# Optimization experiments

Hardware: AMD Instinct MI355X
Metric: run time of the kernel (lower is better)

The kernel has to match this reference:

```python
import jax, jax.numpy as jnp
import numpy as np

B, DIM = 64, 131072


def setup_inputs() -> dict:
    key = jax.random.key(0)
    k1, k2, k3 = jax.random.split(key, 3)
    z = jax.random.normal(k1, (B, DIM), dtype=jnp.float32)
    trace_in = jax.random.normal(k2, (B, DIM), dtype=jnp.float32)
    ctrl = jax.random.normal(k3, (B, 3), dtype=jnp.float32)
    return {"z": z, "trace_in": trace_in, "ctrl": ctrl}


def reference(z, trace_in, ctrl):
    # gates: [B,1]
    store = jax.nn.sigmoid(ctrl[:, 0:1])
    retrieve = jax.nn.sigmoid(ctrl[:, 1:2])
    # clear gate only touches the internal buffer (no effect on outputs); omitted.

    # global max-abs normalization (single scalar, as in torch: z.abs().max())
    z_norm = z / (jnp.abs(z).max() + 1e-6)

    z_f = jnp.fft.fft(z_norm)          # [B,DIM] complex64
    trace_f = jnp.fft.fft(trace_in)    # [B,DIM] complex64
    new_trace_f = trace_f + z_f * store
    new_trace = jnp.fft.ifft(new_trace_f)
    read = jnp.fft.ifft(new_trace_f * jnp.conj(z_f)) * retrieve

    dummy_ptr = jnp.zeros((z.shape[0], 1), dtype=jnp.float32)
    return (read, new_trace, dummy_ptr, jnp.array(1.0, dtype=jnp.float32))
```

## Files before the change

### kernel.cpp

```cpp
#include <hip/hip_runtime.h>
#include <math.h>

#define NROW 64
#define DIM  131072

struct cf { float x, y; };
__device__ __forceinline__ cf cadd(cf a, cf b){ return {a.x+b.x, a.y+b.y}; }
__device__ __forceinline__ cf csub(cf a, cf b){ return {a.x-b.x, a.y-b.y}; }
__device__ __forceinline__ cf cmul(cf a, cf b){ return {a.x*b.x - a.y*b.y, a.x*b.y + a.y*b.x}; }
template<int SG> __device__ __forceinline__ cf muli(cf a){
  return (SG > 0) ? cf{-a.y, a.x} : cf{a.y, -a.x};
}
__device__ __forceinline__ float sigmoidf(float x){ return 1.0f/(1.0f + __expf(-x)); }

__device__ __forceinline__ void wsync(){
  __builtin_amdgcn_wave_barrier();
  asm volatile("" ::: "memory");
}

typedef float __attribute__((ext_vector_type(4))) fvec4;
typedef float __attribute__((ext_vector_type(2))) fvec2;

template<int SG> __device__ __forceinline__ void fft4(cf&a0, cf&a1, cf&a2, cf&a3){
  cf e0=cadd(a0,a2), e1=csub(a0,a2), o0=cadd(a1,a3), o1=csub(a1,a3);
  cf w=muli<SG>(o1);
  a0=cadd(e0,o0); a2=csub(e0,o0); a1=cadd(e1,w); a3=csub(e1,w);
}

template<int SG> __device__ __forceinline__ void fft8(cf v[8]){
  cf e0=v[0], e1=v[2], e2=v[4], e3=v[6];
  cf o0=v[1], o1=v[3], o2=v[5], o3=v[7];
  fft4<SG>(e0,e1,e2,e3); fft4<SG>(o0,o1,o2,o3);
  const float R=0.70710678118654752f;
  cf w1=cmul(o1, cf{R, (float)SG*R});
  cf w2=muli<SG>(o2);
  cf w3=cmul(o3, cf{-R, (float)SG*R});
  v[0]=cadd(e0,o0); v[4]=csub(e0,o0);
  v[1]=cadd(e1,w1); v[5]=csub(e1,w1);
  v[2]=cadd(e2,w2); v[6]=csub(e2,w2);
  v[3]=cadd(e3,w3); v[7]=csub(e3,w3);
}

template<int SG> __device__ __forceinline__ void fft16(cf v[16]){
  cf e[8], o[8];
  #pragma unroll
  for(int i=0;i<8;i++){ e[i]=v[2*i]; o[i]=v[2*i+1]; }
  fft8<SG>(e); fft8<SG>(o);
  const float C[8]={1.f,0.92387953251128674f,0.70710678118654752f,0.38268343236508977f,
                    0.f,-0.38268343236508977f,-0.70710678118654752f,-0.92387953251128674f};
  const float S[8]={0.f,0.38268343236508977f,0.70710678118654752f,0.92387953251128674f,
                    1.f,0.92387953251128674f,0.70710678118654752f,0.38268343236508977f};
  #pragma unroll
  for(int k=0;k<8;k++){
    cf w=cmul(o[k], cf{C[k], (float)SG*S[k]});
    v[k]=cadd(e[k],w); v[k+8]=csub(e[k],w);
  }
}

__global__ void k0_tail(float* __restrict__ dout, int cplx){
  int t = threadIdx.x;
  size_t base = (size_t)2*NROW*DIM*cplx;
  if(t < NROW) dout[base + t] = 0.f;
  else if(t == NROW) dout[base + NROW] = 1.0f;
}

__global__ __launch_bounds__(256) void k1_maxabs(const float* __restrict__ z, unsigned* __restrict__ dst){
  __shared__ float red[256];
  size_t i0 = (size_t)blockIdx.x*blockDim.x + threadIdx.x;
  size_t stride = (size_t)gridDim.x*blockDim.x;
  const float4* z4 = (const float4*)z;
  size_t n4 = (size_t)NROW*DIM/4;
  float m = 0.f;
  for(size_t i=i0;i<n4;i+=stride){
    float4 v=z4[i];
    m = fmaxf(m, fmaxf(fmaxf(fabsf(v.x),fabsf(v.y)), fmaxf(fabsf(v.z),fabsf(v.w))));
  }
  red[threadIdx.x]=m; __syncthreads();
  #pragma unroll
  for(int s=128;s>0;s>>=1){
    if(threadIdx.x<(unsigned)s) red[threadIdx.x]=fmaxf(red[threadIdx.x],red[threadIdx.x+s]);
    __syncthreads();
  }
  if(threadIdx.x==0) atomicMax(dst, __float_as_uint(red[0]));
}

__global__ __launch_bounds__(256) void k2_fwd1(
    const float* __restrict__ z, const float* __restrict__ tr,
    const float* __restrict__ ctrl, const unsigned* __restrict__ maxbits,
    float2* __restrict__ Bws, float* __restrict__ out_nt, int cplx)
{
  __shared__ float reb[4384], imb[4384];
  __shared__ float twc[256], tws[256];
  int t = threadIdx.x;
  int b = blockIdx.x >> 5;
  int n1b = (blockIdx.x & 31) << 4;
  {
    float sv, cv;
    __sincosf(-0.0245436926061703f * (float)t, &sv, &cv);
    twc[t]=cv; tws[t]=sv;
  }
  float s = 1.0f/(__uint_as_float(*maxbits) + 1e-6f);
  float gs = sigmoidf(ctrl[b*3+0]);
  float cc = gs*s;
  const float4* zr4 = (const float4*)(z  + (size_t)b*DIM);
  const float4* tr4 = (const float4*)(tr + (size_t)b*DIM);
  #pragma unroll
  for(int it=0; it<4; ++it){
    int e = t + 256*it;
    int n2 = e >> 2, j4 = e & 3;
    int fi = n2*128 + (n1b>>2) + j4;
    float4 zv = zr4[fi];
    float4 tv = tr4[fi];
    int lb = n2*17 + j4*4;
    reb[lb+0]=zv.x; reb[lb+1]=zv.y; reb[lb+2]=zv.z; reb[lb+3]=zv.w;
    imb[lb+0]=tv.x; imb[lb+1]=tv.y; imb[lb+2]=tv.z; imb[lb+3]=tv.w;
    float n0 = fmaf(cc, zv.x, tv.x);
    float n1v= fmaf(cc, zv.y, tv.y);
    float n2v= fmaf(cc, zv.z, tv.z);
    float n3 = fmaf(cc, zv.w, tv.w);
    size_t n = (size_t)n2*512 + n1b + j4*4;
    size_t oidx = (size_t)b*DIM + n;
    if(cplx == 2){
      fvec4 a  = {n0, 0.f, n1v, 0.f};
      fvec4 bq = {n2v, 0.f, n3, 0.f};
      fvec4* op = (fvec4*)((float2*)out_nt + oidx);
      __builtin_nontemporal_store(a,  op);
      __builtin_nontemporal_store(bq, op+1);
    } else {
      out_nt[oidx+0]=n0; out_nt[oidx+1]=n1v; out_nt[oidx+2]=n2v; out_nt[oidx+3]=n3;
    }
  }
  __syncthreads();
  int f = t & 15, p = t >> 4;
  cf v[16];
  #pragma unroll
  for(int q=0;q<16;q++){ int n2=q*16+p; v[q].x=reb[n2*17+f]; v[q].y=imb[n2*17+f]; }
  fft16<-1>(v);
  #pragma unroll
  for(int kq=1;kq<16;kq++){ int tt=(p*kq)&255; v[kq]=cmul(v[kq], cf{twc[tt], tws[tt]}); }
  __syncthreads();
  #pragma unroll
  for(int kq=0;kq<16;kq++){ reb[f*274 + kq*17 + p]=v[kq].x; imb[f*274 + kq*17 + p]=v[kq].y; }
  __syncthreads();
  #pragma unroll
  for(int pp=0;pp<16;pp++){ v[pp].x=reb[f*274 + p*17 + pp]; v[pp].y=imb[f*274 + p*17 + pp]; }
  fft16<-1>(v);
  int nn1 = n1b + f;
  cf w, st;
  {
    float sv, cv;
    __sincosf(-4.793689960382698e-05f * (float)(nn1*p), &sv, &cv);
    w = {cv, sv};
    __sincosf(-4.793689960382698e-05f * 16.f * (float)nn1, &sv, &cv);
    st = {cv, sv};
  }
  #pragma unroll
  for(int kp=0;kp<16;kp++){
    int k2 = kp*16 + p;
    cf r = cmul(v[kp], w);
    Bws[((size_t)b<<17) + (size_t)k2*512 + nn1] = make_float2(r.x, r.y);
    w = cmul(w, st);
  }
}

template<int SG>
__device__ __forceinline__ void fft512_block(
    float* Xre, float* Xim, float* Tre, float* Tim,
    int lane, const float* twc, const float* tws)
{
  cf v[8];
  #pragma unroll
  for(int q=0;q<8;q++){ v[q].x=Xre[q*64+lane]; v[q].y=Xim[q*64+lane]; }
  fft8<SG>(v);
  #pragma unroll
  for(int kq=1;kq<8;kq++){ int tt=(lane*kq)&511; v[kq]=cmul(v[kq], cf{twc[tt], (float)SG*tws[tt]}); }
  #pragma unroll
  for(int kq=0;kq<8;kq++){ Tre[lane*9+kq]=v[kq].x; Tim[lane*9+kq]=v[kq].y; }
  wsync();
  int kQ = lane>>3, pp = lane&7;
  #pragma unroll
  for(int q=0;q<8;q++){ int idx=(q*8+pp)*9+kQ; v[q].x=Tre[idx]; v[q].y=Tim[idx]; }
  fft8<SG>(v);
  #pragma unroll
  for(int kq=1;kq<8;kq++){ int tt=(pp*kq*8)&511; v[kq]=cmul(v[kq], cf{twc[tt], (float)SG*tws[tt]}); }
  wsync();
  #pragma unroll
  for(int kq=0;kq<8;kq++){ Xre[pp*73+kq*9+kQ]=v[kq].x; Xim[pp*73+kq*9+kQ]=v[kq].y; }
  wsync();
  #pragma unroll
  for(int p2=0;p2<8;p2++){ int idx=p2*73 + kQ*9 + pp; v[p2].x=Xre[idx]; v[p2].y=Xim[idx]; }
  fft8<SG>(v);
  #pragma unroll
  for(int kp=0;kp<8;kp++){ int k=kp*64 + kQ*8 + pp; Tre[k]=v[kp].x; Tim[k]=v[kp].y; }
  wsync();
}

__global__ __launch_bounds__(128) void k3_mid(
    float2* __restrict__ Bws, const float* __restrict__ ctrl,
    const unsigned* __restrict__ maxbits)
{
  __shared__ float Xs[4*584], Ts[4*584];
  __shared__ float twc[512], tws[512];
  int t = threadIdx.x;
  int b  = blockIdx.x >> 7;
  int pr = blockIdx.x & 127;
  int cA = (pr==0) ? 0   : pr;
  int cB = (pr==0) ? 128 : 256-pr;
  int col = t >> 6, lane = t & 63;
  int myc = col ? cB : cA;
  for(int i=t;i<512;i+=128){
    float sv,cv; __sincosf(0.0122718463030851f*(float)i, &sv, &cv);
    twc[i]=cv; tws[i]=sv;
  }
  float s = 1.0f/(__uint_as_float(*maxbits)+1e-6f);
  float gs = sigmoidf(ctrl[b*3+0]);
  float alpha = sigmoidf(ctrl[b*3+1]) * (1.0f/(float)DIM);
  float* Xre = Xs + (2*col)*584; float* Xim = Xre + 584;
  float* Tre = Ts + (2*col)*584; float* Tim = Tre + 584;
  float2* colp = Bws + ((size_t)b<<17) + ((size_t)myc<<9);
  const float4* colp4 = (const float4*)colp;
  #pragma unroll
  for(int r=0;r<4;r++){
    float4 q = colp4[lane + 64*r];
    int j = 2*(lane + 64*r);
    Xre[j]=q.x;   Xim[j]=q.y;
    Xre[j+1]=q.z; Xim[j+1]=q.w;
  }
  __syncthreads();
  fft512_block<-1>(Xre, Xim, Tre, Tim, lane, twc, tws);
  __syncthreads();
  const float* Pre = (pr==0) ? Tre : (Ts + (2*(1-col))*584);
  const float* Pim = Pre + 584;
  #pragma unroll
  for(int r=0;r<8;r++){
    int k1  = lane + 64*r;
    int k1p = (myc==0) ? ((512-k1)&511) : (511-k1);
    float cr = Tre[k1], ci = Tim[k1];
    float qr = Pre[k1p], qi = -Pim[k1p];
    float zur = 0.5f*(cr+qr), zui = 0.5f*(ci+qi);
    float dr = cr-qr, di = ci-qi;
    float tfr = 0.5f*di, tfi = -0.5f*dr;
    float szr = s*zur, szi = s*zui;
    float ntr = fmaf(gs, szr, tfr), nti = fmaf(gs, szi, tfi);
    float prr = (ntr*szr + nti*szi)*alpha;
    float pii = (nti*szr - ntr*szi)*alpha;
    Xre[k1]=prr; Xim[k1]=pii;
  }
  __syncthreads();
  fft512_block<1>(Xre, Xim, Tre, Tim, lane, twc, tws);
  cf w, st;
  {
    float sv,cv;
    __sincosf(4.793689960382698e-05f * (float)(lane*myc), &sv, &cv);
    w = {cv, sv};
    __sincosf(4.793689960382698e-05f * 64.f * (float)myc, &sv, &cv);
    st = {cv, sv};
  }
  #pragma unroll
  for(int r=0;r<8;r++){
    int m1 = lane + 64*r;
    cf r2 = cmul(cf{Tre[m1],Tim[m1]}, w);
    colp[m1] = make_float2(r2.x, r2.y);
    w = cmul(w, st);
  }
}

__global__ __launch_bounds__(256) void k4_inv2(
    const float2* __restrict__ Qws, float* __restrict__ dout, int cplx)
{
  __shared__ float reb[4384], imb[4384];
  __shared__ float twc[256], tws[256];
  int t = threadIdx.x;
  int b = blockIdx.x >> 5;
  int m1b = (blockIdx.x & 31) << 4;
  {
    float sv, cv;
    __sincosf(0.0245436926061703f * (float)t, &sv, &cv);
    twc[t]=cv; tws[t]=sv;
  }
  const float4* Qp = (const float4*)(Qws + ((size_t)b<<17));
  #pragma unroll
  for(int it=0; it<8; ++it){
    int e = t + 256*it;
    int k2 = e >> 3, j = e & 7;
    float4 q = Qp[k2*256 + (m1b>>1) + j];
    int lb = k2*17 + 2*j;
    reb[lb+0]=q.x; imb[lb+0]=q.y;
    reb[lb+1]=q.z; imb[lb+1]=q.w;
  }
  __syncthreads();
  int f = t & 15, p = t >> 4;
  cf v[16];
  #pragma unroll
  for(int q=0;q<16;q++){ int k2=q*16+p; v[q].x=reb[k2*17+f]; v[q].y=imb[k2*17+f]; }
  fft16<1>(v);
  #pragma unroll
  for(int kq=1;kq<16;kq++){ int tt=(p*kq)&255; v[kq]=cmul(v[kq], cf{twc[tt], tws[tt]}); }
  __syncthreads();
  #pragma unroll
  for(int kq=0;kq<16;kq++){ reb[f*274+kq*17+p]=v[kq].x; imb[f*274+kq*17+p]=v[kq].y; }
  __syncthreads();
  #pragma unroll
  for(int pp=0;pp<16;pp++){ v[pp].x=reb[f*274+p*17+pp]; v[pp].y=imb[f*274+p*17+pp]; }
  fft16<1>(v);
  #pragma unroll
  for(int kp=0;kp<16;kp++){
    int m2 = kp*16 + p;
    size_t n = (size_t)(m1b + f) + (size_t)512*m2;
    size_t oidx = (size_t)b*DIM + n;
    if(cplx==2){
      ((float2*)dout)[oidx] = make_float2(v[kp].x, 0.f);
    }
    else dout[oidx] = v[kp].x;
  }
}

extern "C" void kernel_launch(void* const* d_in, const int* in_sizes, int n_in,
                              void* d_out, int out_size, void* d_ws, size_t ws_size,
                              hipStream_t stream)
{
  (void)in_sizes; (void)n_in; (void)ws_size;
  const float* z    = (const float*)d_in[0];
  const float* tr   = (const float*)d_in[1];
  const float* ctrl = (const float*)d_in[2];
  float* dout = (float*)d_out;
  int cplx = (out_size > 20000000) ? 2 : 1;
  unsigned* maxbits = (unsigned*)d_ws;
  float2* Bws = (float2*)((char*)d_ws + 256);

  hipMemsetAsync(d_ws, 0, 4, stream);
  hipLaunchKernelGGL(k0_tail,  dim3(1),    dim3(128), 0, stream, dout, cplx);
  hipLaunchKernelGGL(k1_maxabs,dim3(1024), dim3(256), 0, stream, z, maxbits);
  hipLaunchKernelGGL(k2_fwd1,  dim3(2048), dim3(256), 0, stream,
                     z, tr, ctrl, maxbits, Bws, dout + (size_t)NROW*DIM*cplx, cplx);
  hipLaunchKernelGGL(k3_mid,   dim3(8192), dim3(128), 0, stream, Bws, ctrl, maxbits);
  hipLaunchKernelGGL(k4_inv2,  dim3(2048), dim3(256), 0, stream, Bws, dout, cplx);
}
```

Before: 217.7 us.

## Fuse FFT stages into persistent kernel with per-batch dependency counters

Replaces the three FFT-stage launches with one persistent kernel of 1024 blocks. Each block pulls tiles from an atomic work queue, and per-batch-row completion counters with acquire/release atomics let later stages start on a row as soon as its inputs are ready. This is meant to remove launch gaps and kernel-boundary drains and to overlap stages across rows. It also halves the twiddle table with a sign trick and packs two k3 columns-pairs per 256-thread block. The costs are spin-wait polling, a bounded spin that could proceed early, and shared memory sized for the largest stage, which may lower occupancy.

Measured after the change: 491.4 us. 2.26x slower.

```diff
diff --git a/kernel.cpp b/kernel.cpp
--- a/kernel.cpp
+++ b/kernel.cpp
@@ -3,6 +3,13 @@
 
 #define NROW 64
 #define DIM  131072
+
+#define NK2 2048
+#define NK3 4096
+#define NK4 2048
+#define T_K3 (NK2)
+#define T_K4 (NK2+NK3)
+#define NT_TOT (NK2+NK3+NK4)
 
 struct cf { float x, y; };
 __device__ __forceinline__ cf cadd(cf a, cf b){ return {a.x+b.x, a.y+b.y}; }
@@ -19,7 +26,6 @@
 }
 
 typedef float __attribute__((ext_vector_type(4))) fvec4;
-typedef float __attribute__((ext_vector_type(2))) fvec2;
 
 template<int SG> __device__ __forceinline__ void fft4(cf&a0, cf&a1, cf&a2, cf&a3){
   cf e0=cadd(a0,a2), e1=csub(a0,a2), o0=cadd(a1,a3), o1=csub(a1,a3);
@@ -84,16 +90,35 @@
   if(threadIdx.x==0) atomicMax(dst, __float_as_uint(red[0]));
 }
 
-__global__ __launch_bounds__(256) void k2_fwd1(
+__device__ __forceinline__ void wait_count(unsigned* p, unsigned need){
+  if(threadIdx.x==0){
+    unsigned v, tries = 0;
+    do {
+      v = __hip_atomic_load(p, __ATOMIC_RELAXED, __HIP_MEMORY_SCOPE_AGENT);
+      if(v >= need) break;
+      __builtin_amdgcn_s_sleep(8);
+    } while(++tries < (1u<<19));
+    (void)__hip_atomic_load(p, __ATOMIC_ACQUIRE, __HIP_MEMORY_SCOPE_AGENT);
+  }
+  __syncthreads();
+}
+__device__ __forceinline__ void signal_done(unsigned* p){
+  __syncthreads();
+  if(threadIdx.x==0)
+    (void)__hip_atomic_fetch_add(p, 1u, __ATOMIC_RELEASE, __HIP_MEMORY_SCOPE_AGENT);
+}
+
+
+__device__ __forceinline__ void k2_body(
+    float* __restrict__ S, unsigned tile,
     const float* __restrict__ z, const float* __restrict__ tr,
     const float* __restrict__ ctrl, const unsigned* __restrict__ maxbits,
     float2* __restrict__ Bws, float* __restrict__ out_nt, int cplx)
 {
-  __shared__ float reb[4384], imb[4384];
-  __shared__ float twc[256], tws[256];
+  float* reb = S; float* imb = S+4384; float* twc = S+8768; float* tws = S+9024;
   int t = threadIdx.x;
-  int b = blockIdx.x >> 5;
-  int n1b = (blockIdx.x & 31) << 4;
+  int b = tile >> 5;
+  int n1b = (tile & 31) << 4;
   {
     float sv, cv;
     __sincosf(-0.0245436926061703f * (float)t, &sv, &cv);
@@ -173,7 +198,10 @@
   for(int q=0;q<8;q++){ v[q].x=Xre[q*64+lane]; v[q].y=Xim[q*64+lane]; }
   fft8<SG>(v);
   #pragma unroll
-  for(int kq=1;kq<8;kq++){ int tt=(lane*kq)&511; v[kq]=cmul(v[kq], cf{twc[tt], (float)SG*tws[tt]}); }
+  for(int kq=1;kq<8;kq++){
+    int tt=(lane*kq)&511; int ti=tt&255; float sg=(tt&256)?-1.f:1.f;
+    v[kq]=cmul(v[kq], cf{sg*twc[ti], (float)SG*sg*tws[ti]});
+  }
   #pragma unroll
   for(int kq=0;kq<8;kq++){ Tre[lane*9+kq]=v[kq].x; Tim[lane*9+kq]=v[kq].y; }
   wsync();
@@ -182,7 +210,10 @@
   for(int q=0;q<8;q++){ int idx=(q*8+pp)*9+kQ; v[q].x=Tre[idx]; v[q].y=Tim[idx]; }
   fft8<SG>(v);
   #pragma unroll
-  for(int kq=1;kq<8;kq++){ int tt=(pp*kq*8)&511; v[kq]=cmul(v[kq], cf{twc[tt], (float)SG*tws[tt]}); }
+  for(int kq=1;kq<8;kq++){
+    int tt=(pp*kq*8)&511; int ti=tt&255; float sg=(tt&256)?-1.f:1.f;
+    v[kq]=cmul(v[kq], cf{sg*twc[ti], (float)SG*sg*tws[ti]});
+  }
   wsync();
   #pragma unroll
   for(int kq=0;kq<8;kq++){ Xre[pp*73+kq*9+kQ]=v[kq].x; Xim[pp*73+kq*9+kQ]=v[kq].y; }
@@ -195,45 +226,49 @@
   wsync();
 }
 
-__global__ __launch_bounds__(128) void k3_mid(
+__device__ __forceinline__ void k3_body(
+    float* __restrict__ S, unsigned r,
     float2* __restrict__ Bws, const float* __restrict__ ctrl,
     const unsigned* __restrict__ maxbits)
 {
-  __shared__ float Xs[4*584], Ts[4*584];
-  __shared__ float twc[512], tws[512];
   int t = threadIdx.x;
-  int b  = blockIdx.x >> 7;
-  int pr = blockIdx.x & 127;
+  int b   = r >> 6;
+  int idx = r & 63;
+  int wp  = t >> 7;
+  int tt  = t & 127;
+  int pr  = idx*2 + wp;
   int cA = (pr==0) ? 0   : pr;
   int cB = (pr==0) ? 128 : 256-pr;
-  int col = t >> 6, lane = t & 63;
+  int col = tt >> 6, lane = tt & 63;
   int myc = col ? cB : cA;
-  for(int i=t;i<512;i+=128){
-    float sv,cv; __sincosf(0.0122718463030851f*(float)i, &sv, &cv);
-    twc[i]=cv; tws[i]=sv;
+  int colid = wp*2 + col;
+  float* Xre = S + colid*1168;        float* Xim = Xre + 584;
+  float* Tre = S + 4672 + colid*1168; float* Tim = Tre + 584;
+  float* twc = S + 9344; float* tws = S + 9600;
+  if(t < 256){
+    float sv,cv; __sincosf(0.0122718463030851f*(float)t, &sv, &cv);
+    twc[t]=cv; tws[t]=sv;
   }
   float s = 1.0f/(__uint_as_float(*maxbits)+1e-6f);
   float gs = sigmoidf(ctrl[b*3+0]);
   float alpha = sigmoidf(ctrl[b*3+1]) * (1.0f/(float)DIM);
-  float* Xre = Xs + (2*col)*584; float* Xim = Xre + 584;
-  float* Tre = Ts + (2*col)*584; float* Tim = Tre + 584;
   float2* colp = Bws + ((size_t)b<<17) + ((size_t)myc<<9);
   const float4* colp4 = (const float4*)colp;
   #pragma unroll
-  for(int r=0;r<4;r++){
-    float4 q = colp4[lane + 64*r];
-    int j = 2*(lane + 64*r);
+  for(int rr=0;rr<4;rr++){
+    float4 q = colp4[lane + 64*rr];
+    int j = 2*(lane + 64*rr);
     Xre[j]=q.x;   Xim[j]=q.y;
     Xre[j+1]=q.z; Xim[j+1]=q.w;
   }
   __syncthreads();
   fft512_block<-1>(Xre, Xim, Tre, Tim, lane, twc, tws);
   __syncthreads();
-  const float* Pre = (pr==0) ? Tre : (Ts + (2*(1-col))*584);
+  const float* Pre = (pr==0) ? Tre : (S + 4672 + (wp*2 + (1-col))*1168);
   const float* Pim = Pre + 584;
   #pragma unroll
-  for(int r=0;r<8;r++){
-    int k1  = lane + 64*r;
+  for(int rr=0;rr<8;rr++){
+    int k1  = lane + 64*rr;
     int k1p = (myc==0) ? ((512-k1)&511) : (511-k1);
     float cr = Tre[k1], ci = Tim[k1];
     float qr = Pre[k1p], qi = -Pim[k1p];
@@ -257,22 +292,22 @@
     st = {cv, sv};
   }
   #pragma unroll
-  for(int r=0;r<8;r++){
-    int m1 = lane + 64*r;
+  for(int rr=0;rr<8;rr++){
+    int m1 = lane + 64*rr;
     cf r2 = cmul(cf{Tre[m1],Tim[m1]}, w);
     colp[m1] = make_float2(r2.x, r2.y);
     w = cmul(w, st);
   }
 }
 
-__global__ __launch_bounds__(256) void k4_inv2(
+__device__ __forceinline__ void k4_body(
+    float* __restrict__ S, unsigned r,
     const float2* __restrict__ Qws, float* __restrict__ dout, int cplx)
 {
-  __shared__ float reb[4384], imb[4384];
-  __shared__ float twc[256], tws[256];
+  float* reb = S; float* imb = S+4384; float* twc = S+8768; float* tws = S+9024;
   int t = threadIdx.x;
-  int b = blockIdx.x >> 5;
-  int m1b = (blockIdx.x & 31) << 4;
+  int b = r >> 5;
+  int m1b = (r & 31) << 4;
   {
     float sv, cv;
     __sincosf(0.0245436926061703f * (float)t, &sv, &cv);
@@ -308,10 +343,41 @@
     int m2 = kp*16 + p;
     size_t n = (size_t)(m1b + f) + (size_t)512*m2;
     size_t oidx = (size_t)b*DIM + n;
-    if(cplx==2){
-      ((float2*)dout)[oidx] = make_float2(v[kp].x, 0.f);
+    if(cplx==2) ((float2*)dout)[oidx] = make_float2(v[kp].x, 0.f);
+    else dout[oidx] = v[kp].x;
+  }
+}
+
+__global__ __launch_bounds__(256) void mega(
+    const float* __restrict__ z, const float* __restrict__ tr,
+    const float* __restrict__ ctrl, const unsigned* __restrict__ maxbits,
+    float2* __restrict__ Bws, float* __restrict__ out_nt,
+    float* __restrict__ dout, int cplx, unsigned* __restrict__ syncw)
+{
+  __shared__ float S[9856];
+  __shared__ unsigned tk_s;
+  unsigned* qhead  = syncw;
+  unsigned* k2done = syncw + 1;
+  unsigned* k3done = syncw + 65;
+  for(;;){
+    __syncthreads();
+    if(threadIdx.x==0) tk_s = atomicAdd(qhead, 1u);
+    __syncthreads();
+    unsigned tk = tk_s;
+    if(tk >= NT_TOT) break;
+    if(tk < T_K3){
+      k2_body(S, tk, z, tr, ctrl, maxbits, Bws, out_nt, cplx);
+      signal_done(&k2done[tk>>5]);
+    } else if(tk < T_K4){
+      unsigned r = tk - T_K3;
+      wait_count(&k2done[r>>6], 32);
+      k3_body(S, r, Bws, ctrl, maxbits);
+      signal_done(&k3done[r>>6]);
+    } else {
+      unsigned r = tk - T_K4;
+      wait_count(&k3done[r>>5], 64);
+      k4_body(S, r, Bws, dout, cplx);
     }
-    else dout[oidx] = v[kp].x;
   }
 }
 
@@ -327,12 +393,13 @@
   int cplx = (out_size > 20000000) ? 2 : 1;
   unsigned* maxbits = (unsigned*)d_ws;
   float2* Bws = (float2*)((char*)d_ws + 256);
+  unsigned* syncw = (unsigned*)((char*)d_ws + 256 + (size_t)NROW*DIM*8);
 
   hipMemsetAsync(d_ws, 0, 4, stream);
+  hipMemsetAsync(syncw, 0, 640, stream);
   hipLaunchKernelGGL(k0_tail,  dim3(1),    dim3(128), 0, stream, dout, cplx);
   hipLaunchKernelGGL(k1_maxabs,dim3(1024), dim3(256), 0, stream, z, maxbits);
-  hipLaunchKernelGGL(k2_fwd1,  dim3(2048), dim3(256), 0, stream,
-                     z, tr, ctrl, maxbits, Bws, dout + (size_t)NROW*DIM*cplx, cplx);
-  hipLaunchKernelGGL(k3_mid,   dim3(8192), dim3(128), 0, stream, Bws, ctrl, maxbits);
-  hipLaunchKernelGGL(k4_inv2,  dim3(2048), dim3(256), 0, stream, Bws, dout, cplx);
-}
+  hipLaunchKernelGGL(mega,     dim3(1024), dim3(256), 0, stream,
+                     z, tr, ctrl, maxbits, Bws, dout + (size_t)NROW*DIM*cplx,
+                     dout, cplx, syncw);
+}
```
